# Kernel tuning notes

Hardware: AMD Instinct MI355X
Metric: run time of the kernel (lower is better)

The kernel has to match this reference:

```python
import jax, jax.numpy as jnp
import numpy as np

KH = KW = 3
K = KH * KW
STRIDE = 1
PAD = 1
DIL = 1
GROUPS = 1
DG = 1  # deformable_groups
CIN = 256
COUT = 256
DC = 64  # depth_channels


def conv2d(x, w, b):
    out = jax.lax.conv_general_dilated(
        x, w, (STRIDE, STRIDE), [(PAD, PAD), (PAD, PAD)],
        rhs_dilation=(DIL, DIL), dimension_numbers=('NCHW', 'OIHW', 'NCHW'))
    return out + b[None, :, None, None]


def deform_sample(x, offset, mask):
    """Modulated deformable im2col. x:[N,C,H,W], offset:[N,DG*2*K,Ho,Wo],
    mask:[N,DG*K,Ho,Wo] or None. Returns cols [N,C,K,Ho,Wo]."""
    N, C, H, W = x.shape
    Ho = (H + 2 * PAD - (DIL * (KH - 1) + 1)) // STRIDE + 1
    Wo = (W + 2 * PAD - (DIL * (KW - 1) + 1)) // STRIDE + 1
    ky, kx = jnp.meshgrid(jnp.arange(KH), jnp.arange(KW), indexing='ij')
    # base sampling grid per kernel tap: [K,Ho,Wo]
    base_y = (jnp.arange(Ho) * STRIDE - PAD)[None, :, None] + (ky.reshape(-1) * DIL)[:, None, None]
    base_x = (jnp.arange(Wo) * STRIDE - PAD)[None, None, :] + (kx.reshape(-1) * DIL)[:, None, None]
    off = offset.reshape(N, DG, K, 2, Ho, Wo)  # [...,0]=dy, [...,1]=dx (CUDA layout)
    y = base_y[None, None].astype(x.dtype) + off[:, :, :, 0]
    xx = base_x[None, None].astype(x.dtype) + off[:, :, :, 1]
    y0 = jnp.floor(y)
    x0 = jnp.floor(xx)
    ly = y - y0
    lx = xx - x0
    y0i = y0.astype(jnp.int32)
    x0i = x0.astype(jnp.int32)
    xg = x.reshape(N, DG, C // DG, H * W)

    def gather(iy, ix):
        valid = ((iy >= 0) & (iy < H) & (ix >= 0) & (ix < W)).astype(x.dtype)
        idx = (jnp.clip(iy, 0, H - 1) * W + jnp.clip(ix, 0, W - 1)).reshape(N, DG, 1, K * Ho * Wo)
        v = jnp.take_along_axis(xg, idx, axis=3).reshape(N, DG, C // DG, K, Ho, Wo)
        return v * valid[:, :, None]

    v00 = gather(y0i, x0i)
    v01 = gather(y0i, x0i + 1)
    v10 = gather(y0i + 1, x0i)
    v11 = gather(y0i + 1, x0i + 1)
    w00 = (1 - ly) * (1 - lx)
    w01 = (1 - ly) * lx
    w10 = ly * (1 - lx)
    w11 = ly * lx
    cols = (v00 * w00[:, :, None] + v01 * w01[:, :, None]
            + v10 * w10[:, :, None] + v11 * w11[:, :, None])
    if mask is not None:
        cols = cols * mask.reshape(N, DG, 1, K, Ho, Wo)
    return cols.reshape(N, C, K, Ho, Wo)


def deform_conv2d(x, offset, mask, weight, bias):
    cols = deform_sample(x, offset, mask)  # [N,C,K,Ho,Wo]
    N, C, _, Ho, Wo = cols.shape
    Cout = weight.shape[0]
    cg = C // GROUPS
    cols = cols.reshape(N, GROUPS, cg * K, Ho * Wo)
    wg = weight.reshape(GROUPS, Cout // GROUPS, cg * K)
    out = jnp.einsum('gok,ngkp->ngop', wg, cols).reshape(N, Cout, Ho, Wo)
    return out + bias[None, :, None, None]


def setup_inputs() -> dict:
    key = jax.random.key(0)
    ks = jax.random.split(key, 8)
    x = jax.random.normal(ks[0], (4, CIN, 64, 64), dtype=jnp.float32)
    depth = jax.random.normal(ks[1], (4, DC, 64, 64), dtype=jnp.float32)
    stdv = 1.0 / np.sqrt(CIN * KH * KW)
    weight = jax.random.uniform(ks[2], (COUT, CIN // GROUPS, KH, KW), minval=-stdv, maxval=stdv, dtype=jnp.float32)
    bias = jnp.zeros((COUT,), jnp.float32)
    # offset/mask convs are zero-init in the module; use small random weights
    # so the irregular gather path is actually exercised.
    off_w = 0.05 * jax.random.normal(ks[3], (DG * 2 * K, CIN + DC, KH, KW), dtype=jnp.float32)
    off_b = 0.05 * jax.random.normal(ks[4], (DG * 2 * K,), dtype=jnp.float32)
    mask_w = 0.05 * jax.random.normal(ks[5], (DG * K, DC, KH, KW), dtype=jnp.float32)
    mask_b = 0.05 * jax.random.normal(ks[6], (DG * K,), dtype=jnp.float32)
    return {"x": x, "depth": depth, "weight": weight, "bias": bias,
            "off_w": off_w, "off_b": off_b, "mask_w": mask_w, "mask_b": mask_b}


def reference(x, depth, weight, bias, off_w, off_b, mask_w, mask_b):
    # offset = conv_offset(cat(x, depth))
    offset = conv2d(jnp.concatenate([x, depth], axis=1), off_w, off_b)
    # mask = sigmoid(DeformConv(depth, offset))  (non-modulated deform conv)
    mask = jax.nn.sigmoid(deform_conv2d(depth, offset, None, mask_w, mask_b))
    # modulated deformable conv on x
    return deform_conv2d(x, offset, mask, weight, bias)
```

## Files before the change

### kernel.cpp

```cpp
#include <hip/hip_runtime.h>


typedef __bf16 bf16x8 __attribute__((ext_vector_type(8)));
typedef float f32x4 __attribute__((ext_vector_type(4)));
typedef float float2_u __attribute__((ext_vector_type(2), aligned(4)));

__device__ __forceinline__ unsigned short f2bf(float f) {
  unsigned b = __float_as_uint(f);
  return (unsigned short)((b + 0x7fffu + ((b >> 16) & 1u)) >> 16);
}

__global__ __launch_bounds__(1024) void k_offset_all(
    const float* __restrict__ x, const float* __restrict__ depth,
    const float* __restrict__ w, const float* __restrict__ off_w,
    const float* __restrict__ off_b,
    unsigned short* __restrict__ wbf, float* __restrict__ offs)
{
  const int tid = threadIdx.x;
  for (int i = blockIdx.x * 1024 + tid; i < 589824; i += 262144)
    wbf[i] = f2bf(w[i]);

  const int n = blockIdx.x >> 6, ho = blockIdx.x & 63;
  const int lane = tid & 63;
  const int wave = tid >> 6;

  float acc[18];
#pragma unroll
  for (int i = 0; i < 18; ++i) acc[i] = 0.f;

  const int c0 = __builtin_amdgcn_readfirstlane(wave * 20);

  for (int ci = 0; ci < 20; ++ci) {
    const int c = c0 + ci;
    const float* p = (c < 256) ? (x + (((n << 8) + c) << 12))
                               : (depth + (((n << 6) + (c - 256)) << 12));
    const float v0 = (ho > 0)  ? p[((ho - 1) << 6) + lane] : 0.f;
    const float v1 =             p[( ho      << 6) + lane];
    const float v2 = (ho < 63) ? p[((ho + 1) << 6) + lane] : 0.f;

    float v[9];
#pragma unroll
    for (int ky = 0; ky < 3; ++ky) {
      const float r = (ky == 0) ? v0 : ((ky == 1) ? v1 : v2);
#pragma unroll
      for (int kx = 0; kx < 3; ++kx) {
        const int src = lane + kx - 1;
        const float s = __shfl(r, src & 63);
        v[ky * 3 + kx] = (src >= 0 && src < 64) ? s : 0.f;
      }
    }
    const float* wp = off_w + c * 9;
#pragma unroll
    for (int co = 0; co < 18; ++co) {
      const float* ww = wp + co * 2880;
#pragma unroll
      for (int t = 0; t < 9; ++t) acc[co] += v[t] * ww[t];
    }
  }

  __shared__ float red[16][18][64];
#pragma unroll
  for (int co = 0; co < 18; ++co) red[wave][co][lane] = acc[co];
  __syncthreads();
  for (int o = tid; o < 18 * 64; o += 1024) {
    const int co = o >> 6, wo = o & 63;
    float s = off_b[co];
#pragma unroll
    for (int wv = 0; wv < 16; ++wv) s += red[wv][co][wo];
    offs[((n * 18 + co) << 12) + (ho << 6) + wo] = s;
  }
}

__device__ __forceinline__ void stage_channel_row(const float* src, char* dstb,
                                                  int lane) {
  const char* s = (const char*)src + lane * 4;
#pragma unroll
  for (int j = 0; j < 32; ++j)
    __builtin_amdgcn_global_load_lds(
        (const __attribute__((address_space(1))) void*)(s + j * 256),
        (__attribute__((address_space(3))) void*)(dstb + j * 272), 4, 0, 0);
}

__global__ __launch_bounds__(512, 2) void k_fused_gemm(
    const float* __restrict__ x, const float* __restrict__ depth,
    const float* __restrict__ offs, const float* __restrict__ mask_w,
    const float* __restrict__ mask_b, const unsigned short* __restrict__ wbf,
    const float* __restrict__ bias, float* __restrict__ out)
{
  __shared__ __align__(16) char pool[101376];
  char* stripc = pool;
  unsigned short (*Bs)[72]  = (unsigned short (*)[72])(pool + 78336);
  float4 (*pwT)[64]         = (float4 (*)[64])(pool + 87552);
  int (*piT)[64]            = (int (*)[64])(pool + 96768);
  float (*mskL)[64]         = (float (*)[64])(pool + 99072);
  float (*red)[9][64]       = (float (*)[9][64])(pool + 78336);

  const int tid = threadIdx.x;
  const int b    = blockIdx.x;
  const int xcd  = b & 7, bslot = b >> 3;
  const int n    = xcd >> 1;
  const int ho   = ((xcd & 1) << 5) + bslot;
  const int pxb  = ho << 6;
  const int ylo  = min(max(ho - 15, 0), 32);

  const int pxl  = tid & 63;
  const int oct  = tid >> 6;
  const int lane = tid & 63;
  const int mrow = lane & 15;
  const int koct = lane >> 4;
  const float* xn = x + ((long)(n << 8) << 12);

  stage_channel_row(xn + (oct << 12) + (ylo << 6), stripc + oct * 8704, lane);
  int c_staged = 8;

  {
    const int wo = lane;
    int ia[9], ib[9];
    float w0[9], w1[9], w2c[9], w3[9];
    const float* op = offs + ((n * 18) << 12) + (ho << 6) + wo;
#pragma unroll
    for (int k = 0; k < 9; ++k) {
      const float dy = op[(2 * k) << 12];
      const float dx = op[(2 * k + 1) << 12];
      const float yy = (float)(ho - 1 + k / 3) + dy;
      const float xx = (float)(wo - 1 + k % 3) + dx;
      const float y0f = floorf(yy), x0f = floorf(xx);
      const float ly = yy - y0f, lx = xx - x0f;
      const int y0 = (int)y0f, x0 = (int)x0f;
      const int y0c = min(max(y0, 0), 63);
      const int y1c = min(max(y0 + 1, 0), 63);
      const float fy0 = (y0 >= 0 && y0 < 64) ? 1.f : 0.f;
      const float fy1 = (y0 >= -1 && y0 < 63) ? 1.f : 0.f;
      const int x0c = min(max(x0, 0), 63);
      const int x1c = min(max(x0 + 1, 0), 63);
      const int bx  = min(max(x0, 0), 62);
      const float vx0 = (x0 >= 0 && x0 < 64) ? 1.f : 0.f;
      const float vx1 = (x0 >= -1 && x0 < 63) ? 1.f : 0.f;
      const float wl = (1.f - lx) * vx0 * ((x0c == bx) ? 1.f : 0.f)
                     + lx * vx1 * ((x1c == bx) ? 1.f : 0.f);
      const float wr = (1.f - lx) * vx0 * ((x0c == bx + 1) ? 1.f : 0.f)
                     + lx * vx1 * ((x1c == bx + 1) ? 1.f : 0.f);
      const float a0 = (1.f - ly) * fy0;
      const float a1 = ly * fy1;
      ia[k] = ((y0c << 6) + bx) << 2;
      ib[k] = ((y1c << 6) + bx) << 2;
      w0[k] = wl * a0;  w1[k] = wr * a0;
      w2c[k] = wl * a1; w3[k] = wr * a1;
    }

    float acc2[9];
#pragma unroll
    for (int i = 0; i < 9; ++i) acc2[i] = 0.f;

    const int cbase = __builtin_amdgcn_readfirstlane(oct * 8);
    for (int cc = 0; cc < 8; ++cc) {
      const int c = cbase + cc;
      const char* p = (const char*)(depth + (((n << 6) + c) << 12));
      float val[9];
#pragma unroll
      for (int k = 0; k < 9; ++k) {
        const float2_u A = *(const float2_u*)(p + ia[k]);
        const float2_u B = *(const float2_u*)(p + ib[k]);
        val[k] = A.x * w0[k] + A.y * w1[k] + B.x * w2c[k] + B.y * w3[k];
      }
      const float* wp = mask_w + c * 9;
#pragma unroll
      for (int co = 0; co < 9; ++co) {
#pragma unroll
        for (int k = 0; k < 9; ++k) acc2[co] += val[k] * wp[co * 576 + k];
      }
    }
#pragma unroll
    for (int co = 0; co < 9; ++co) red[oct][co][lane] = acc2[co];
  }
  __syncthreads();

  for (int o = tid; o < 576; o += 512) {
    const int co = o >> 6, wo = o & 63;
    float s = mask_b[co];
#pragma unroll
    for (int wv = 0; wv < 8; ++wv) s += red[wv][co][wo];
    mskL[co][wo] = 1.f / (1.f + expf(-s));
  }
  __syncthreads();

  for (int e = tid; e < 576; e += 512) {
    const int tap = e >> 6, pl = e & 63;
    const int wo = pl;
    const float dy = offs[((n * 18 + 2 * tap) << 12) + pxb + pl];
    const float dx = offs[((n * 18 + 2 * tap + 1) << 12) + pxb + pl];
    const float m  = mskL[tap][pl];
    const float yy = (float)(ho - 1 + tap / 3) + dy;
    const float xx = (float)(wo - 1 + tap % 3) + dx;
    const float y0f = floorf(yy), x0f = floorf(xx);
    const float ly = yy - y0f, lx = xx - x0f;
    const int y0 = (int)y0f, x0 = (int)x0f;
    const int y0c = min(max(y0, 0), 63);
    const int y1c = min(max(y0 + 1, 0), 63);
    const float fy0 = (y0 >= 0 && y0 < 64) ? 1.f : 0.f;
    const float fy1 = (y0 >= -1 && y0 < 63) ? 1.f : 0.f;
    const int x0c = min(max(x0, 0), 63);
    const int x1c = min(max(x0 + 1, 0), 63);
    const int bx  = min(max(x0, 0), 62);
    const float vx0 = (x0 >= 0 && x0 < 64) ? 1.f : 0.f;
    const float vx1 = (x0 >= -1 && x0 < 63) ? 1.f : 0.f;
    const float wl = (1.f - lx) * vx0 * ((x0c == bx) ? 1.f : 0.f)
                   + lx * vx1 * ((x1c == bx) ? 1.f : 0.f);
    const float wr = (1.f - lx) * vx0 * ((x0c == bx + 1) ? 1.f : 0.f)
                   + lx * vx1 * ((x1c == bx + 1) ? 1.f : 0.f);
    const float a0 = (1.f - ly) * fy0 * m;
    const float a1 = ly * fy1 * m;
    pwT[tap][pl] = make_float4(wl * a0, wr * a0, wl * a1, wr * a1);
    const int ry0 = y0c - ylo, ry1 = y1c - ylo;
    const int ry0c = min(max(ry0, 0), 31), ry1c = min(max(ry1, 0), 31);
    const int bad = ((ry0 != ry0c) || (ry1 != ry1c)) ? 1 : 0;
    const int ad0 = ry0c * 272 + (bx << 2);
    const int ad1 = ry1c * 272 + (bx << 2);
    piT[tap][pl] = ad0 | (ad1 << 14) | (bad << 28);
  }
  __syncthreads();

  auto gather = [&](int ic) {
    const int k0 = (ic << 6) + (oct << 3);
    const int c0 = (int)(((unsigned)k0 * 7282u) >> 16);
    int tap = k0 - 9 * c0;
    const int s9 = (int)(((unsigned)c0 * 7282u) >> 16);
    int soff = (c0 - 9 * s9) * 8704;

    __align__(16) unsigned short v[8];
    unsigned badm = 0;
#pragma unroll
    for (int j = 0; j < 8; ++j) {
      const int pk  = piT[tap][pxl];
      const float4 w = pwT[tap][pxl];
      const float2_u A = *(const float2_u*)(stripc + soff + (pk & 16383));
      const float2_u B = *(const float2_u*)(stripc + soff + ((pk >> 14) & 16383));
      v[j] = f2bf(A.x * w.x + A.y * w.y + B.x * w.z + B.y * w.w);
      badm |= ((unsigned)pk >> 28) << j;
      if (++tap == 9) {
        tap = 0;
        soff += 8704; if (soff == 9 * 8704) soff = 0;
      }
    }

    if (__builtin_expect(badm != 0, 0)) {
#pragma unroll
      for (int j = 0; j < 8; ++j) if (badm & (1u << j)) {
        const int k = k0 + j;
        const int c = (int)(((unsigned)k * 7282u) >> 16);
        const int tp = k - 9 * c;
        const float dy = offs[((n * 18 + 2 * tp) << 12) + pxb + pxl];
        const float dx = offs[((n * 18 + 2 * tp + 1) << 12) + pxb + pxl];
        const float m  = mskL[tp][pxl];
        const float yy = (float)(ho - 1 + tp / 3) + dy;
        const float xx = (float)(pxl - 1 + tp % 3) + dx;
        const float y0f = floorf(yy), x0f = floorf(xx);
        const float ly = yy - y0f, lx = xx - x0f;
        const int y0 = (int)y0f, x0 = (int)x0f;
        const int y0c = min(max(y0, 0), 63);
        const int y1c = min(max(y0 + 1, 0), 63);
        const float fy0 = (y0 >= 0 && y0 < 64) ? 1.f : 0.f;
        const float fy1 = (y0 >= -1 && y0 < 63) ? 1.f : 0.f;
        const int x0c = min(max(x0, 0), 63);
        const int x1c = min(max(x0 + 1, 0), 63);
        const int bx  = min(max(x0, 0), 62);
        const float vx0 = (x0 >= 0 && x0 < 64) ? 1.f : 0.f;
        const float vx1 = (x0 >= -1 && x0 < 63) ? 1.f : 0.f;
        const float wl = (1.f - lx) * vx0 * ((x0c == bx) ? 1.f : 0.f)
                       + lx * vx1 * ((x1c == bx) ? 1.f : 0.f);
        const float wr = (1.f - lx) * vx0 * ((x0c == bx + 1) ? 1.f : 0.f)
                       + lx * vx1 * ((x1c == bx + 1) ? 1.f : 0.f);
        const float a0 = (1.f - ly) * fy0 * m;
        const float a1 = ly * fy1 * m;
        const char* pg = (const char*)xn + ((long)c << 14);
        const float2_u Ag = *(const float2_u*)(pg + (((y0c << 6) + bx) << 2));
        const float2_u Bg = *(const float2_u*)(pg + (((y1c << 6) + bx) << 2));
        v[j] = f2bf(Ag.x * (wl * a0) + Ag.y * (wr * a0) +
                    Bg.x * (wl * a1) + Bg.y * (wr * a1));
      }
    }
    *(int4*)&Bs[pxl][oct << 3] = *(const int4*)v;
  };

  bf16x8 afc[2][2];
#pragma unroll
  for (int mt = 0; mt < 2; ++mt)
#pragma unroll
    for (int ks = 0; ks < 2; ++ks) {
      const int row = (oct << 5) + (mt << 4) + mrow;
      const int col = (ks << 5) + (koct << 3);
      afc[mt][ks] = *(const bf16x8*)(wbf + row * 2304 + col);
    }

  gather(0);
  __syncthreads();

  f32x4 acc[2][4];
#pragma unroll
  for (int mt = 0; mt < 2; ++mt)
#pragma unroll
    for (int nt = 0; nt < 4; ++nt)
#pragma unroll
      for (int r = 0; r < 4; ++r) acc[mt][nt][r] = 0.f;

  for (int ic = 0; ic < 36; ++ic) {
    if (ic < 35) {
      const int c_end = (64 * ic + 127) / 9;
      const int cw = c_staged + oct;
      if (cw <= c_end) {
        const int slt = cw - 9 * (int)(((unsigned)cw * 7282u) >> 16);
        stage_channel_row(xn + (cw << 12) + (ylo << 6),
                          stripc + slt * 8704, lane);
      }
      c_staged = c_end + 1;
    }

    bf16x8 afn[2][2];
    if (ic < 35) {
      const int kc = (ic + 1) << 6;
#pragma unroll
      for (int mt = 0; mt < 2; ++mt)
#pragma unroll
        for (int ks = 0; ks < 2; ++ks) {
          const int row = (oct << 5) + (mt << 4) + mrow;
          const int col = kc + (ks << 5) + (koct << 3);
          afn[mt][ks] = *(const bf16x8*)(wbf + row * 2304 + col);
        }
    }

#pragma unroll
    for (int ks = 0; ks < 2; ++ks)
#pragma unroll
      for (int nt = 0; nt < 4; ++nt) {
        const bf16x8 bfr =
            *(const bf16x8*)&Bs[(nt << 4) + mrow][(ks << 5) + (koct << 3)];
        acc[0][nt] = __builtin_amdgcn_mfma_f32_16x16x32_bf16(afc[0][ks], bfr,
                                                             acc[0][nt], 0, 0, 0);
        acc[1][nt] = __builtin_amdgcn_mfma_f32_16x16x32_bf16(afc[1][ks], bfr,
                                                             acc[1][nt], 0, 0, 0);
      }

    __syncthreads();
    if (ic < 35) gather(ic + 1);
    __syncthreads();

#pragma unroll
    for (int mt = 0; mt < 2; ++mt)
#pragma unroll
      for (int ks = 0; ks < 2; ++ks) afc[mt][ks] = afn[mt][ks];
  }

#pragma unroll
  for (int mt = 0; mt < 2; ++mt)
#pragma unroll
    for (int nt = 0; nt < 4; ++nt)
#pragma unroll
      for (int r = 0; r < 4; ++r) {
        const int co = (oct << 5) + (mt << 4) + ((lane >> 4) << 2) + r;
        const int pxg = pxb + (nt << 4) + (lane & 15);
        out[(((n << 8) + co) << 12) + pxg] = acc[mt][nt][r] + bias[co];
      }
}

extern "C" void kernel_launch(void* const* d_in, const int* in_sizes, int n_in,
                              void* d_out, int out_size, void* d_ws, size_t ws_size,
                              hipStream_t stream) {
  const float* x      = (const float*)d_in[0];
  const float* depth  = (const float*)d_in[1];
  const float* weight = (const float*)d_in[2];
  const float* bias   = (const float*)d_in[3];
  const float* off_w  = (const float*)d_in[4];
  const float* off_b  = (const float*)d_in[5];
  const float* mask_w = (const float*)d_in[6];
  const float* mask_b = (const float*)d_in[7];
  float* out = (float*)d_out;

  float* offs = (float*)d_ws;
  unsigned short* wbf = (unsigned short*)(offs + 294912);

  k_offset_all<<<256, 1024, 0, stream>>>(x, depth, weight, off_w, off_b,
                                         wbf, offs);
  k_fused_gemm<<<256, 512, 0, stream>>>(x, depth, offs, mask_w, mask_b,
                                        wbf, bias, out);
}
```

Baseline: 235.6 us.

## Transpose offset-conv weights in prep kernel and broadcast via readlane with prefetch

Moves the bf16 weight conversion into a new prep kernel that also transposes the offset-conv weights to a per-channel contiguous layout. The offset kernel now loads each channel's 162 weights as three coalesced per-lane loads and broadcasts them with readlane instead of issuing scalar or uniform loads per tap. It also software-prefetches the next channel's input rows and weights. This adds an extra kernel launch and a workspace buffer, and it raises register pressure in the 1024-thread kernel.

```diff
diff --git a/kernel.cpp b/kernel.cpp
--- a/kernel.cpp
+++ b/kernel.cpp
@@ -10,16 +10,29 @@
   return (unsigned short)((b + 0x7fffu + ((b >> 16) & 1u)) >> 16);
 }
 
+__device__ __forceinline__ float rdlane(float v, int l) {
+  return __int_as_float(__builtin_amdgcn_readlane(__float_as_int(v), l));
+}
+
+__global__ __launch_bounds__(256) void k_prep(
+    const float* __restrict__ w, const float* __restrict__ off_w,
+    unsigned short* __restrict__ wbf, float* __restrict__ off_wT)
+{
+  const int i = blockIdx.x * 256 + threadIdx.x;
+  wbf[i] = f2bf(w[i]);
+  if (i < 51840) {
+    const unsigned c = (unsigned)i / 162u, r = (unsigned)i - c * 162u;
+    const unsigned co = r / 9u, t = r - co * 9u;
+    off_wT[i] = off_w[co * 2880 + c * 9 + t];
+  }
+}
+
 __global__ __launch_bounds__(1024) void k_offset_all(
     const float* __restrict__ x, const float* __restrict__ depth,
-    const float* __restrict__ w, const float* __restrict__ off_w,
-    const float* __restrict__ off_b,
-    unsigned short* __restrict__ wbf, float* __restrict__ offs)
+    const float* __restrict__ off_wT, const float* __restrict__ off_b,
+    float* __restrict__ offs)
 {
   const int tid = threadIdx.x;
-  for (int i = blockIdx.x * 1024 + tid; i < 589824; i += 262144)
-    wbf[i] = f2bf(w[i]);
-
   const int n = blockIdx.x >> 6, ho = blockIdx.x & 63;
   const int lane = tid & 63;
   const int wave = tid >> 6;
@@ -30,18 +43,35 @@
 
   const int c0 = __builtin_amdgcn_readfirstlane(wave * 20);
 
-  for (int ci = 0; ci < 20; ++ci) {
-    const int c = c0 + ci;
+  auto loadrows = [&](int c, float& a, float& b, float& d) {
     const float* p = (c < 256) ? (x + (((n << 8) + c) << 12))
                                : (depth + (((n << 6) + (c - 256)) << 12));
-    const float v0 = (ho > 0)  ? p[((ho - 1) << 6) + lane] : 0.f;
-    const float v1 =             p[( ho      << 6) + lane];
-    const float v2 = (ho < 63) ? p[((ho + 1) << 6) + lane] : 0.f;
+    a = (ho > 0)  ? p[((ho - 1) << 6) + lane] : 0.f;
+    b =             p[( ho      << 6) + lane];
+    d = (ho < 63) ? p[((ho + 1) << 6) + lane] : 0.f;
+  };
+  auto loadw = [&](int c, float& wa, float& wb, float& wc) {
+    const float* wt = off_wT + c * 162;
+    wa = wt[lane];
+    wb = wt[64 + lane];
+    wc = wt[128 + lane];
+  };
+
+  float r0, r1, r2, w0v, w1v, w2v;
+  loadrows(c0, r0, r1, r2);
+  loadw(c0, w0v, w1v, w2v);
+
+  for (int ci = 0; ci < 20; ++ci) {
+    float n0, n1, n2, m0, m1, m2;
+    if (ci < 19) {
+      loadrows(c0 + ci + 1, n0, n1, n2);
+      loadw(c0 + ci + 1, m0, m1, m2);
+    }
 
     float v[9];
 #pragma unroll
     for (int ky = 0; ky < 3; ++ky) {
-      const float r = (ky == 0) ? v0 : ((ky == 1) ? v1 : v2);
+      const float r = (ky == 0) ? r0 : ((ky == 1) ? r1 : r2);
 #pragma unroll
       for (int kx = 0; kx < 3; ++kx) {
         const int src = lane + kx - 1;
@@ -49,13 +79,22 @@
         v[ky * 3 + kx] = (src >= 0 && src < 64) ? s : 0.f;
       }
     }
-    const float* wp = off_w + c * 9;
+
 #pragma unroll
     for (int co = 0; co < 18; ++co) {
-      const float* ww = wp + co * 2880;
-#pragma unroll
-      for (int t = 0; t < 9; ++t) acc[co] += v[t] * ww[t];
-    }
+#pragma unroll
+      for (int t = 0; t < 9; ++t) {
+        constexpr int dummy = 0; (void)dummy;
+        const int f = co * 9 + t;
+        const float wv = (f < 64)  ? rdlane(w0v, f)
+                       : (f < 128) ? rdlane(w1v, f - 64)
+                                   : rdlane(w2v, f - 128);
+        acc[co] += v[t] * wv;
+      }
+    }
+
+    r0 = n0; r1 = n1; r2 = n2;
+    w0v = m0; w1v = m1; w2v = m2;
   }
 
   __shared__ float red[16][18][64];
@@ -377,9 +416,10 @@
 
   float* offs = (float*)d_ws;
   unsigned short* wbf = (unsigned short*)(offs + 294912);
-
-  k_offset_all<<<256, 1024, 0, stream>>>(x, depth, weight, off_w, off_b,
-                                         wbf, offs);
+  float* off_wT = (float*)(wbf + 589824);
+
+  k_prep<<<2304, 256, 0, stream>>>(weight, off_w, wbf, off_wT);
+  k_offset_all<<<256, 1024, 0, stream>>>(x, depth, off_wT, off_b, offs);
   k_fused_gemm<<<256, 512, 0, stream>>>(x, depth, offs, mask_w, mask_b,
                                         wbf, bias, out);
 }
```

Measured after the change: 238.2 us. Within noise of the previous version (+1.1%).

## Compute offset conv with split-bf16 MFMA GEMM and separate weight prep kernel

Applied to the files above, without the earlier changes.

Replaces the scalar FP32 shuffle-based offset convolution with an implicit GEMM on bf16 MFMA, using a hi/lo bf16 split of weights and activations (three MFMAs per step) to keep near-FP32 accuracy. Weight conversion to bf16 moves into a separate prep kernel that also pads and splits the offset weights. This aims to cut the FMA-bound cost of the offset conv, in exchange for an extra launch, im2col building in LDS with per-element gathers, and three times the MFMA work.

```diff
diff --git a/kernel.cpp b/kernel.cpp
--- a/kernel.cpp
+++ b/kernel.cpp
@@ -9,65 +9,111 @@
   unsigned b = __float_as_uint(f);
   return (unsigned short)((b + 0x7fffu + ((b >> 16) & 1u)) >> 16);
 }
-
-__global__ __launch_bounds__(1024) void k_offset_all(
+__device__ __forceinline__ float bf2f(unsigned short h) {
+  return __uint_as_float((unsigned)h << 16);
+}
+
+__global__ __launch_bounds__(256) void k_prep(
+    const float* __restrict__ w, const float* __restrict__ off_w,
+    unsigned short* __restrict__ wbf, unsigned short* __restrict__ wo_hi,
+    unsigned short* __restrict__ wo_lo)
+{
+  const int i = blockIdx.x * 256 + threadIdx.x;
+  wbf[i] = f2bf(w[i]);
+  if (i < 92160) {
+    const int co = i / 2880;
+    const float wv = (co < 18) ? off_w[i] : 0.f;
+    const unsigned short hi = f2bf(wv);
+    wo_hi[i] = hi;
+    wo_lo[i] = f2bf(wv - bf2f(hi));
+  }
+}
+
+__global__ __launch_bounds__(512) void k_offset_gemm(
     const float* __restrict__ x, const float* __restrict__ depth,
-    const float* __restrict__ w, const float* __restrict__ off_w,
-    const float* __restrict__ off_b,
-    unsigned short* __restrict__ wbf, float* __restrict__ offs)
+    const unsigned short* __restrict__ wo_hi,
+    const unsigned short* __restrict__ wo_lo,
+    const float* __restrict__ off_b, float* __restrict__ offs)
 {
-  const int tid = threadIdx.x;
-  for (int i = blockIdx.x * 1024 + tid; i < 589824; i += 262144)
-    wbf[i] = f2bf(w[i]);
-
-  const int n = blockIdx.x >> 6, ho = blockIdx.x & 63;
+  __shared__ __align__(16) unsigned short BsH[64][104];
+  __shared__ __align__(16) unsigned short BsL[64][104];
+
+  const int tid  = threadIdx.x;
+  const int n    = blockIdx.x >> 6, ho = blockIdx.x & 63;
   const int lane = tid & 63;
-  const int wave = tid >> 6;
-
-  float acc[18];
-#pragma unroll
-  for (int i = 0; i < 18; ++i) acc[i] = 0.f;
-
-  const int c0 = __builtin_amdgcn_readfirstlane(wave * 20);
-
-  for (int ci = 0; ci < 20; ++ci) {
-    const int c = c0 + ci;
-    const float* p = (c < 256) ? (x + (((n << 8) + c) << 12))
-                               : (depth + (((n << 6) + (c - 256)) << 12));
-    const float v0 = (ho > 0)  ? p[((ho - 1) << 6) + lane] : 0.f;
-    const float v1 =             p[( ho      << 6) + lane];
-    const float v2 = (ho < 63) ? p[((ho + 1) << 6) + lane] : 0.f;
-
-    float v[9];
-#pragma unroll
-    for (int ky = 0; ky < 3; ++ky) {
-      const float r = (ky == 0) ? v0 : ((ky == 1) ? v1 : v2);
-#pragma unroll
-      for (int kx = 0; kx < 3; ++kx) {
-        const int src = lane + kx - 1;
-        const float s = __shfl(r, src & 63);
-        v[ky * 3 + kx] = (src >= 0 && src < 64) ? s : 0.f;
-      }
-    }
-    const float* wp = off_w + c * 9;
-#pragma unroll
-    for (int co = 0; co < 18; ++co) {
-      const float* ww = wp + co * 2880;
-#pragma unroll
-      for (int t = 0; t < 9; ++t) acc[co] += v[t] * ww[t];
-    }
-  }
-
-  __shared__ float red[16][18][64];
-#pragma unroll
-  for (int co = 0; co < 18; ++co) red[wave][co][lane] = acc[co];
-  __syncthreads();
-  for (int o = tid; o < 18 * 64; o += 1024) {
-    const int co = o >> 6, wo = o & 63;
-    float s = off_b[co];
-#pragma unroll
-    for (int wv = 0; wv < 16; ++wv) s += red[wv][co][wo];
-    offs[((n * 18 + co) << 12) + (ho << 6) + wo] = s;
+  const int wv   = tid >> 6;
+  const int mt   = wv >> 2;
+  const int nt   = wv & 3;
+  const int mrow = lane & 15;
+  const int koct = lane >> 4;
+  const int px   = lane;
+
+  auto build = [&](int kc) {
+    __align__(8) unsigned short vh[12], vl[12];
+#pragma unroll
+    for (int j = 0; j < 12; ++j) {
+      const int k  = kc + wv * 12 + j;
+      const int c  = (int)(((unsigned)k * 7282u) >> 16);
+      const int tap = k - 9 * c;
+      const int ky = tap / 3, kx = tap - 3 * ky;
+      const int yr = ho - 1 + ky;
+      const int xc = px - 1 + kx;
+      const float* p = (c < 256) ? (x + (((n << 8) + c) << 12))
+                                 : (depth + (((n << 6) + (c - 256)) << 12));
+      const int yrc = min(max(yr, 0), 63), xcc = min(max(xc, 0), 63);
+      const float f = (((unsigned)yr < 64u) && ((unsigned)xc < 64u)) ? 1.f : 0.f;
+      const float val = p[(yrc << 6) + xcc] * f;
+      const unsigned short hi = f2bf(val);
+      vh[j] = hi;
+      vl[j] = f2bf(val - bf2f(hi));
+    }
+    *(int2*)&BsH[px][wv * 12]     = *(const int2*)&vh[0];
+    *(int2*)&BsH[px][wv * 12 + 4] = *(const int2*)&vh[4];
+    *(int2*)&BsH[px][wv * 12 + 8] = *(const int2*)&vh[8];
+    *(int2*)&BsL[px][wv * 12]     = *(const int2*)&vl[0];
+    *(int2*)&BsL[px][wv * 12 + 4] = *(const int2*)&vl[4];
+    *(int2*)&BsL[px][wv * 12 + 8] = *(const int2*)&vl[8];
+  };
+
+  f32x4 acc;
+#pragma unroll
+  for (int r = 0; r < 4; ++r) acc[r] = 0.f;
+
+  const int arow = ((mt << 4) + mrow) * 2880;
+  const unsigned short* ah = wo_hi + arow;
+  const unsigned short* al = wo_lo + arow;
+  const int brow = (nt << 4) + mrow;
+
+  for (int st = 0; st < 30; ++st) {
+    const int kc = st * 96;
+    bf16x8 afh[3], afl[3];
+#pragma unroll
+    for (int q = 0; q < 3; ++q) {
+      afh[q] = *(const bf16x8*)(ah + kc + q * 32 + (koct << 3));
+      afl[q] = *(const bf16x8*)(al + kc + q * 32 + (koct << 3));
+    }
+
+    build(kc);
+    __syncthreads();
+
+#pragma unroll
+    for (int q = 0; q < 3; ++q) {
+      const bf16x8 bh = *(const bf16x8*)&BsH[brow][q * 32 + (koct << 3)];
+      const bf16x8 bl = *(const bf16x8*)&BsL[brow][q * 32 + (koct << 3)];
+      acc = __builtin_amdgcn_mfma_f32_16x16x32_bf16(afh[q], bh, acc, 0, 0, 0);
+      acc = __builtin_amdgcn_mfma_f32_16x16x32_bf16(afh[q], bl, acc, 0, 0, 0);
+      acc = __builtin_amdgcn_mfma_f32_16x16x32_bf16(afl[q], bh, acc, 0, 0, 0);
+    }
+    __syncthreads();
+  }
+
+#pragma unroll
+  for (int r = 0; r < 4; ++r) {
+    const int co = (mt << 4) + ((lane >> 4) << 2) + r;
+    if (co < 18) {
+      const int wo = (nt << 4) + (lane & 15);
+      offs[((n * 18 + co) << 12) + (ho << 6) + wo] = acc[r] + off_b[co];
+    }
   }
 }
 
@@ -377,9 +423,11 @@
 
   float* offs = (float*)d_ws;
   unsigned short* wbf = (unsigned short*)(offs + 294912);
-
-  k_offset_all<<<256, 1024, 0, stream>>>(x, depth, weight, off_w, off_b,
-                                         wbf, offs);
+  unsigned short* wo_hi = wbf + 589824;
+  unsigned short* wo_lo = wo_hi + 92160;
+
+  k_prep<<<2304, 256, 0, stream>>>(weight, off_w, wbf, wo_hi, wo_lo);
+  k_offset_gemm<<<256, 512, 0, stream>>>(x, depth, wo_hi, wo_lo, off_b, offs);
   k_fused_gemm<<<256, 512, 0, stream>>>(x, depth, offs, mask_w, mask_b,
                                         wbf, bias, out);
 }
```

New measurement: 266.9 us. 1.13x slower.
